# Kernel optimization log

Hardware: AMD Instinct MI355X
Metric: run time of the kernel (lower is better)

Reference implementation:

```python
import jax, jax.numpy as jnp
import numpy as np

B, S, D, H, DK, DFF = 4, 1024, 1024, 16, 64, 4096
EPS = 1e-5


def layer_norm(x, g, b):
    m = jnp.mean(x, axis=-1, keepdims=True)
    v = jnp.var(x, axis=-1, keepdims=True)
    return (x - m) * jax.lax.rsqrt(v + EPS) * g + b


def setup_inputs() -> dict:
    key = jax.random.key(0)
    ks = jax.random.split(key, 12)
    sc = 0.02
    return {
        "x":    jax.random.normal(ks[0], (B, S, D), jnp.float32),
        # per-head Q/K/V projections, stacked over heads: [H, D, DK]
        "Wq":   jax.random.normal(ks[1], (H, D, DK), jnp.float32) * sc,
        "bq":   jnp.zeros((H, DK), jnp.float32),
        "Wk":   jax.random.normal(ks[2], (H, D, DK), jnp.float32) * sc,
        "bk":   jnp.zeros((H, DK), jnp.float32),
        "Wv":   jax.random.normal(ks[3], (H, D, DK), jnp.float32) * sc,
        "bv":   jnp.zeros((H, DK), jnp.float32),
        # output projection: [H*DK, D]
        "Wo":   jax.random.normal(ks[4], (H * DK, D), jnp.float32) * sc,
        "bo":   jnp.zeros((D,), jnp.float32),
        # FFN
        "W1":   jax.random.normal(ks[5], (D, DFF), jnp.float32) * sc,
        "b1":   jnp.zeros((DFF,), jnp.float32),
        "W2":   jax.random.normal(ks[6], (DFF, D), jnp.float32) * sc,
        "b2":   jnp.zeros((D,), jnp.float32),
        # LayerNorms
        "g1":   jnp.ones((D,), jnp.float32),
        "be1":  jnp.zeros((D,), jnp.float32),
        "g2":   jnp.ones((D,), jnp.float32),
        "be2":  jnp.zeros((D,), jnp.float32),
    }


def reference(x, Wq, bq, Wk, bk, Wv, bv, Wo, bo, W1, b1, W2, b2, g1, be1, g2, be2):
    # batched multi-head attention (original loops per head; math identical)
    q = jnp.einsum("bsd,hdk->bhsk", x, Wq) + bq[None, :, None, :]
    k = jnp.einsum("bsd,hdk->bhsk", x, Wk) + bk[None, :, None, :]
    v = jnp.einsum("bsd,hdk->bhsk", x, Wv) + bv[None, :, None, :]
    scale = 1.0 / jnp.sqrt(jnp.asarray(DK, x.dtype))
    scores = jnp.einsum("bhsk,bhtk->bhst", q * scale, k)
    attn = jax.nn.softmax(scores, axis=-1)  # dropout = eval-mode identity
    o = jnp.einsum("bhst,bhtk->bhsk", attn, v)
    # torch.cat over heads along dim 2 -> [B, S, H*DK]
    o = jnp.transpose(o, (0, 2, 1, 3)).reshape(B, S, H * DK)
    att = o @ Wo + bo
    # post-attn: residual of LayerNorm(att)
    x = x + layer_norm(att, g1, be1)
    # FFN
    pos = jax.nn.relu(x @ W1 + b1) @ W2 + b2
    x = x + layer_norm(pos, g2, be2)
    return x
```

## Files before the change

### kernel.cpp

```cpp
#include <hip/hip_runtime.h>
#include <hip/hip_bf16.h>
#include <hip/hip_fp16.h>

typedef unsigned short u16;
typedef short bf16x8_t __attribute__((ext_vector_type(8)));
typedef float f32x4_t  __attribute__((ext_vector_type(4)));

__device__ __forceinline__ u16 f2bf(float f) {
    __hip_bfloat16 h = __float2bfloat16(f);
    union { __hip_bfloat16 b; u16 u; } cv; cv.b = h; return cv.u;
}

__device__ __forceinline__ float bf2f(u16 u) {
    union { unsigned int w; float f; } cv; cv.w = (unsigned int)u << 16; return cv.f;
}

__device__ __forceinline__ void g2l16(const void* g, void* l) {
    __builtin_amdgcn_global_load_lds(
        (const __attribute__((address_space(1))) unsigned int*)g,
        (__attribute__((address_space(3))) unsigned int*)l, 16, 0, 0);
}

__global__ __launch_bounds__(256)
void k_prep(const float* __restrict__ x, u16* __restrict__ Xb,
            const float* __restrict__ Wq, const float* __restrict__ Wk,
            const float* __restrict__ Wv, u16* __restrict__ Wqkvt,
            const float* __restrict__ Wo, const float* __restrict__ W1,
            const float* __restrict__ W2, u16* __restrict__ Wot,
            u16* __restrict__ W1t, u16* __restrict__ W2t)
{
    int id = blockIdx.x;
    if (id < 4096) {
        int i = id * 256 + threadIdx.x;
        float4 f = ((const float4*)x)[i];
        ushort4 o;
        o.x = f2bf(f.x); o.y = f2bf(f.y); o.z = f2bf(f.z); o.w = f2bf(f.w);
        ((ushort4*)Xb)[i] = o;
        return;
    }
    id -= 4096;
    const float* in; u16* out; int R, C, r0, c0;
    if (id < 768) {
        int zx = id >> 8, hy = (id >> 4) & 15, tx = id & 15;
        in  = (zx == 0 ? Wq : (zx == 1 ? Wk : Wv)) + (size_t)hy * 65536;
        out = Wqkvt + ((size_t)zx * 1024 + hy * 64) * 1024;
        R = 1024; C = 64; r0 = tx * 64; c0 = 0;
    } else {
        id -= 768;
        int tx, ty;
        if (id < 256)       { in = Wo; out = Wot; R = 1024; C = 1024; tx = id & 15; ty = id >> 4; }
        else if (id < 1280) { id -= 256; in = W1; out = W1t; R = 1024; C = 4096; tx = id & 63; ty = id >> 6; }
        else                { id -= 1280; in = W2; out = W2t; R = 4096; C = 1024; tx = id & 15; ty = id >> 4; }
        r0 = ty * 64; c0 = tx * 64;
    }
    __shared__ float t[64][65];
    int lc = threadIdx.x & 63, lr = threadIdx.x >> 6;
#pragma unroll
    for (int p = 0; p < 16; ++p) {
        int rr = p * 4 + lr;
        t[rr][lc] = in[(size_t)(r0 + rr) * C + c0 + lc];
    }
    __syncthreads();
#pragma unroll
    for (int p = 0; p < 16; ++p) {
        int cc = p * 4 + lr;
        out[(size_t)(c0 + cc) * R + r0 + lc] = f2bf(t[lc][cc]);
    }
}

__global__ __launch_bounds__(256, 4)
void k_gemm_bt(const u16* __restrict__ A, const u16* __restrict__ Bt,
               void* __restrict__ out, int M, int N, int K, int kchunk)
{
    __shared__ __align__(16) u16 As[2 * 128 * 32];
    __shared__ __align__(16) u16 Bs[2 * 128 * 32];
    int tid = threadIdx.x;
    int wave = tid >> 6, lane = tid & 63;

    int nx = gridDim.x, nwg = nx * gridDim.y;
    int f  = blockIdx.x + nx * blockIdx.y;
    int f2 = (f & 7) * (nwg >> 3) + (f >> 3);
    int bx = f2 % nx, by = f2 / nx;
    int row0 = by * 128, col0 = bx * 128;

    int z = blockIdx.z;
    int kbeg = z * kchunk;

    int lrow = lane >> 2, lcol = (lane & 3) * 8;
    const u16* pA0 = A  + (size_t)(row0 + wave * 16 + lrow) * K + kbeg + lcol;
    const u16* pA1 = pA0 + (size_t)64 * K;
    const u16* pB0 = Bt + (size_t)(col0 + wave * 16 + lrow) * K + kbeg + lcol;
    const u16* pB1 = pB0 + (size_t)64 * K;
    u16* lA0 = &As[wave * 512];
    u16* lA1 = &As[2048 + wave * 512];
    u16* lB0 = &Bs[wave * 512];
    u16* lB1 = &Bs[2048 + wave * 512];

    int wm = (wave >> 1) * 64, wn = (wave & 1) * 64;
    int quad = lane >> 4, l16 = lane & 15;

    f32x4_t acc[4][4];
#pragma unroll
    for (int i = 0; i < 4; i++)
#pragma unroll
        for (int j = 0; j < 4; j++) acc[i][j] = f32x4_t{0.f, 0.f, 0.f, 0.f};

    for (int kk = 0; kk < kchunk; kk += 64) {
        __syncthreads();
        g2l16(pA0, lA0);      g2l16(pA1, lA1);
        g2l16(pA0 + 32, lA0 + 4096); g2l16(pA1 + 32, lA1 + 4096);
        g2l16(pB0, lB0);      g2l16(pB1, lB1);
        g2l16(pB0 + 32, lB0 + 4096); g2l16(pB1 + 32, lB1 + 4096);
        pA0 += 64; pA1 += 64; pB0 += 64; pB1 += 64;
        __syncthreads();

#pragma unroll
        for (int s = 0; s < 2; ++s) {
            const u16* as = &As[s * 4096];
            const u16* bs = &Bs[s * 4096];
            bf16x8_t a[4], b[4];
#pragma unroll
            for (int i = 0; i < 4; ++i)
                a[i] = *(const bf16x8_t*)&as[(wm + i * 16 + l16) * 32 + quad * 8];
#pragma unroll
            for (int j = 0; j < 4; ++j)
                b[j] = *(const bf16x8_t*)&bs[(wn + j * 16 + l16) * 32 + quad * 8];
#pragma unroll
            for (int i = 0; i < 4; ++i)
#pragma unroll
                for (int j = 0; j < 4; ++j)
                    acc[i][j] = __builtin_amdgcn_mfma_f32_16x16x32_bf16(a[i], b[j], acc[i][j], 0, 0, 0);
        }
    }

#pragma unroll
    for (int i = 0; i < 4; ++i)
#pragma unroll
        for (int j = 0; j < 4; ++j)
#pragma unroll
            for (int r = 0; r < 4; ++r) {
                int row = row0 + wm + i * 16 + quad * 4 + r;
                int col = col0 + wn + j * 16 + l16;
                ((__half*)out)[(size_t)z * M * N + (size_t)row * N + col] =
                    __float2half(acc[i][j][r]);
            }
}

template<int EPI>
__device__ __forceinline__
void gemm256x128(const u16* __restrict__ A, const u16* __restrict__ Bt,
                 const float* __restrict__ bias0, void* __restrict__ out,
                 int M, int N, int K, int kchunk, int z, int bx, int by)
{
    __shared__ __align__(16) u16 As[2 * 256 * 32];
    __shared__ __align__(16) u16 Bs[2 * 128 * 32];
    int tid = threadIdx.x;
    int wave = tid >> 6, lane = tid & 63;
    int row0 = by * 256, col0 = bx * 128;
    int kbeg = z * kchunk;

    int lrow = lane >> 2, lcol = (lane & 3) * 8;
    const u16* pA0 = A  + (size_t)(row0 + wave * 16 + lrow) * K + kbeg + lcol;
    const u16* pA1 = pA0 + (size_t)128 * K;
    const u16* pB0 = Bt + (size_t)(col0 + wave * 16 + lrow) * K + kbeg + lcol;
    u16* lA0 = &As[wave * 512];
    u16* lA1 = &As[4096 + wave * 512];
    u16* lB0 = &Bs[wave * 512];

    int wm = (wave >> 1) * 64, wn = (wave & 1) * 64;
    int quad = lane >> 4, l16 = lane & 15;

    f32x4_t acc[4][4];
#pragma unroll
    for (int i = 0; i < 4; i++)
#pragma unroll
        for (int j = 0; j < 4; j++) acc[i][j] = f32x4_t{0.f, 0.f, 0.f, 0.f};

    for (int kk = 0; kk < kchunk; kk += 64) {
        __syncthreads();
        g2l16(pA0, lA0);           g2l16(pA1, lA1);
        g2l16(pA0 + 32, lA0 + 8192); g2l16(pA1 + 32, lA1 + 8192);
        g2l16(pB0, lB0);           g2l16(pB0 + 32, lB0 + 4096);
        pA0 += 64; pA1 += 64; pB0 += 64;
        __syncthreads();

#pragma unroll
        for (int s = 0; s < 2; ++s) {
            const u16* as = &As[s * 8192];
            const u16* bs = &Bs[s * 4096];
            bf16x8_t a[4], b[4];
#pragma unroll
            for (int i = 0; i < 4; ++i)
                a[i] = *(const bf16x8_t*)&as[(wm + i * 16 + l16) * 32 + quad * 8];
#pragma unroll
            for (int j = 0; j < 4; ++j)
                b[j] = *(const bf16x8_t*)&bs[(wn + j * 16 + l16) * 32 + quad * 8];
#pragma unroll
            for (int i = 0; i < 4; ++i)
#pragma unroll
                for (int j = 0; j < 4; ++j)
                    acc[i][j] = __builtin_amdgcn_mfma_f32_16x16x32_bf16(a[i], b[j], acc[i][j], 0, 0, 0);
        }
    }

#pragma unroll
    for (int i = 0; i < 4; ++i)
#pragma unroll
        for (int j = 0; j < 4; ++j)
#pragma unroll
            for (int r = 0; r < 4; ++r) {
                int row = row0 + wm + i * 16 + quad * 4 + r;
                int col = col0 + wn + j * 16 + l16;
                float v = acc[i][j][r];
                if (EPI == 0) {
                    ((__half*)out)[(size_t)z * M * N + (size_t)row * N + col] = __float2half(v);
                } else {
                    ((u16*)out)[(size_t)row * N + col] = f2bf(fmaxf(v + bias0[col], 0.f));
                }
            }
}

__global__ __launch_bounds__(256, 4)
void k_gemm_qkv(const u16* __restrict__ A, const u16* __restrict__ Bt,
                const float* __restrict__ bq, const float* __restrict__ bk,
                const float* __restrict__ bv, u16* __restrict__ QK,
                u16* __restrict__ VT, int M, int N, int K)
{
    __shared__ __align__(16) char pool[34816];
    u16* As = (u16*)pool;
    u16* Bs = (u16*)(pool + 16384);

    int tid = threadIdx.x;
    int wave = tid >> 6, lane = tid & 63;

    int nx = gridDim.x, nwg = nx * gridDim.y;
    int f  = blockIdx.x + nx * blockIdx.y;
    int f2 = (f & 7) * (nwg >> 3) + (f >> 3);
    int bx = f2 % nx, by = f2 / nx;
    int row0 = by * 128, col0 = bx * 128;

    int lrow = lane >> 2, lcol = (lane & 3) * 8;
    const u16* pA0 = A  + (size_t)(row0 + wave * 16 + lrow) * K + lcol;
    const u16* pA1 = pA0 + (size_t)64 * K;
    const u16* pB0 = Bt + (size_t)(col0 + wave * 16 + lrow) * K + lcol;
    const u16* pB1 = pB0 + (size_t)64 * K;
    u16* lA0 = As + wave * 512;
    u16* lA1 = As + 2048 + wave * 512;
    u16* lB0 = Bs + wave * 512;
    u16* lB1 = Bs + 2048 + wave * 512;

    int wm = (wave >> 1) * 64, wn = (wave & 1) * 64;
    int quad = lane >> 4, l16 = lane & 15;

    f32x4_t acc[4][4];
#pragma unroll
    for (int i = 0; i < 4; i++)
#pragma unroll
        for (int j = 0; j < 4; j++) acc[i][j] = f32x4_t{0.f, 0.f, 0.f, 0.f};

    for (int kk = 0; kk < K; kk += 64) {
        __syncthreads();
        g2l16(pA0, lA0);      g2l16(pA1, lA1);
        g2l16(pA0 + 32, lA0 + 4096); g2l16(pA1 + 32, lA1 + 4096);
        g2l16(pB0, lB0);      g2l16(pB1, lB1);
        g2l16(pB0 + 32, lB0 + 4096); g2l16(pB1 + 32, lB1 + 4096);
        pA0 += 64; pA1 += 64; pB0 += 64; pB1 += 64;
        __syncthreads();

#pragma unroll
        for (int s = 0; s < 2; ++s) {
            const u16* as = As + s * 4096;
            const u16* bs = Bs + s * 4096;
            bf16x8_t a[4], b[4];
#pragma unroll
            for (int i = 0; i < 4; ++i)
                a[i] = *(const bf16x8_t*)(as + (wm + i * 16 + l16) * 32 + quad * 8);
#pragma unroll
            for (int j = 0; j < 4; ++j)
                b[j] = *(const bf16x8_t*)(bs + (wn + j * 16 + l16) * 32 + quad * 8);
#pragma unroll
            for (int i = 0; i < 4; ++i)
#pragma unroll
                for (int j = 0; j < 4; ++j)
                    acc[i][j] = __builtin_amdgcn_mfma_f32_16x16x32_bf16(a[i], b[j], acc[i][j], 0, 0, 0);
        }
    }

    int proj = col0 >> 10;
    int h0   = (col0 & 1023) >> 6;
    int b_   = row0 >> 10, sb = row0 & 1023;

    if (proj < 2) {
        const float* bp = proj == 0 ? bq : bk;
        float scale = proj == 0 ? 0.18033688f : 1.f;
        u16* dstbase = QK + (size_t)proj * 4194304;
#pragma unroll
        for (int i = 0; i < 4; ++i)
#pragma unroll
            for (int j = 0; j < 4; ++j)
#pragma unroll
                for (int r = 0; r < 4; ++r) {
                    int row = row0 + wm + i * 16 + quad * 4 + r;
                    int col = col0 + wn + j * 16 + l16;
                    int within = col & 1023;
                    float v = (acc[i][j][r] + bp[within]) * scale;
                    int h = within >> 6, kq = within & 63;
                    int s_ = row & 1023;
                    size_t bh = (size_t)((b_ << 4) + h);
                    dstbase[bh * 65536 + ((size_t)s_ << 6) + kq] = f2bf(v);
                }
    } else {
        u16* tile = (u16*)pool;
        __syncthreads();
#pragma unroll
        for (int i = 0; i < 4; ++i)
#pragma unroll
            for (int j = 0; j < 4; ++j) {
                int c = wn + j * 16 + l16;
                int bcol = (col0 & 1023) + c;
#pragma unroll
                for (int r = 0; r < 4; ++r)
                    tile[c * 136 + wm + i * 16 + quad * 4 + r] =
                        f2bf(acc[i][j][r] + bv[bcol]);
            }
        __syncthreads();
        int c = tid >> 1, v0 = (tid & 1) * 8;
        int head = c >> 6, kq = c & 63;
        size_t bh = (size_t)(b_ * 16 + h0 + head);
        u16* vb = VT + bh * 65536 + (size_t)kq * 1024 + sb;
#pragma unroll
        for (int k = 0; k < 8; ++k) {
            uint4 x = *(const uint4*)&tile[c * 136 + (v0 + k) * 8];
            *(uint4*)&vb[(v0 + k) * 8] = x;
        }
    }
}

__global__ __launch_bounds__(512, 4)
void k_gemm_ffn1(const u16* __restrict__ A, const u16* __restrict__ Bt,
                 const float* __restrict__ b1, void* __restrict__ out,
                 int M, int N, int K)
{
    int nx = gridDim.x, nwg = nx * gridDim.y;
    int f  = blockIdx.x + nx * blockIdx.y;
    int f2 = (f & 7) * (nwg >> 3) + (f >> 3);
    gemm256x128<1>(A, Bt, b1, out, M, N, K, K, 0, f2 % nx, f2 / nx);
}

__global__ __launch_bounds__(512, 4)
void k_gemm_ffn2(const u16* __restrict__ A, const u16* __restrict__ Bt,
                 void* __restrict__ out, int M, int N, int K, int kchunk)
{
    int nx = gridDim.x, nwg = nx * gridDim.y;
    int f  = blockIdx.x + nx * blockIdx.y;
    int f2 = (f & 7) * (nwg >> 3) + (f >> 3);
    gemm256x128<0>(A, Bt, nullptr, out, M, N, K, kchunk, blockIdx.z, f2 % nx, f2 / nx);
}

__global__ __launch_bounds__(512, 4)
void k_attn(const u16* __restrict__ Qg, const u16* __restrict__ Kg,
            const u16* __restrict__ VTg, u16* __restrict__ Og)
{
    __shared__ __align__(16) u16 Ks[2][64 * 64];
    __shared__ __align__(16) u16 Vs[2][64 * 64];
    __shared__ __align__(16) u16 Ps[128 * 64];

    int tid = threadIdx.x, wave = tid >> 6, lane = tid & 63;
    int quad = lane >> 4, l16 = lane & 15;

    int f  = blockIdx.x + gridDim.x * blockIdx.y;
    int f2 = (f & 7) * ((gridDim.x * gridDim.y) >> 3) + (f >> 3);
    int bh = f2 >> 3;
    int q0 = (f2 & 7) * 128;
    int wrow = wave * 16;

    const u16* Qp  = Qg  + (size_t)bh * 65536;
    const u16* Kp  = Kg  + (size_t)bh * 65536;
    const u16* VTp = VTg + (size_t)bh * 65536;

    int arow_g = q0 + wrow + l16;
    bf16x8_t aq0 = *(const bf16x8_t*)&Qp[(size_t)arow_g * 64 + quad * 8];
    bf16x8_t aq1 = *(const bf16x8_t*)&Qp[(size_t)arow_g * 64 + 32 + quad * 8];

    int srow = tid >> 3, scb = tid & 7;
    int sdoff = srow * 64 + ((scb ^ (srow & 7)) * 8);

    uint4 kreg = *(const uint4*)&Kp[(size_t)srow * 64 + scb * 8];
    uint4 vreg = *(const uint4*)&VTp[(size_t)srow * 1024 + scb * 8];

    f32x4_t o[4], lsum;
#pragma unroll
    for (int nt = 0; nt < 4; ++nt) o[nt] = f32x4_t{0.f, 0.f, 0.f, 0.f};
    lsum = f32x4_t{0.f, 0.f, 0.f, 0.f};

    bf16x8_t ones;
#pragma unroll
    for (int j = 0; j < 8; ++j) ones[j] = (short)0x3F80;

    int a7 = l16 & 7;

    *(uint4*)&Ks[0][sdoff] = kreg;
    *(uint4*)&Vs[0][sdoff] = vreg;
    kreg = *(const uint4*)&Kp[(size_t)(64 + srow) * 64 + scb * 8];
    vreg = *(const uint4*)&VTp[(size_t)srow * 1024 + 64 + scb * 8];
    __syncthreads();

    for (int t = 0; t < 16; ++t) {
        int cur = t & 1, nxt = cur ^ 1;
        if (t < 15) {
            *(uint4*)&Ks[nxt][sdoff] = kreg;
            *(uint4*)&Vs[nxt][sdoff] = vreg;
        }
        if (t < 14) {
            kreg = *(const uint4*)&Kp[(size_t)((t + 2) * 64 + srow) * 64 + scb * 8];
            vreg = *(const uint4*)&VTp[(size_t)srow * 1024 + (t + 2) * 64 + scb * 8];
        }

        f32x4_t s[4];
        __builtin_amdgcn_s_setprio(1);
#pragma unroll
        for (int nt = 0; nt < 4; ++nt) {
            int brow = nt * 16 + l16;
            bf16x8_t bk0 = *(const bf16x8_t*)&Ks[cur][brow * 64 + ((quad ^ a7) * 8)];
            bf16x8_t bk1 = *(const bf16x8_t*)&Ks[cur][brow * 64 + (((4 + quad) ^ a7) * 8)];
            s[nt] = __builtin_amdgcn_mfma_f32_16x16x32_bf16(aq0, bk0, f32x4_t{0.f,0.f,0.f,0.f}, 0, 0, 0);
            s[nt] = __builtin_amdgcn_mfma_f32_16x16x32_bf16(aq1, bk1, s[nt], 0, 0, 0);
        }
        __builtin_amdgcn_s_setprio(0);

#pragma unroll
        for (int nt = 0; nt < 4; ++nt) {
            int pcb = nt * 2 + (l16 >> 3);
#pragma unroll
            for (int r = 0; r < 4; ++r) {
                float p = exp2f(s[nt][r]);
                int pr = wrow + quad * 4 + r;
                Ps[pr * 64 + ((pcb ^ (pr & 7)) * 8) + (l16 & 7)] = f2bf(p);
            }
        }

        int arow = wrow + l16;
        bf16x8_t ap0 = *(const bf16x8_t*)&Ps[arow * 64 + ((quad ^ a7) * 8)];
        bf16x8_t ap1 = *(const bf16x8_t*)&Ps[arow * 64 + (((4 + quad) ^ a7) * 8)];
        __builtin_amdgcn_s_setprio(1);
#pragma unroll
        for (int nt = 0; nt < 4; ++nt) {
            int vrow = nt * 16 + l16;
            bf16x8_t bv0 = *(const bf16x8_t*)&Vs[cur][vrow * 64 + ((quad ^ a7) * 8)];
            bf16x8_t bv1 = *(const bf16x8_t*)&Vs[cur][vrow * 64 + (((4 + quad) ^ a7) * 8)];
            o[nt] = __builtin_amdgcn_mfma_f32_16x16x32_bf16(ap0, bv0, o[nt], 0, 0, 0);
            o[nt] = __builtin_amdgcn_mfma_f32_16x16x32_bf16(ap1, bv1, o[nt], 0, 0, 0);
        }
        lsum = __builtin_amdgcn_mfma_f32_16x16x32_bf16(ap0, ones, lsum, 0, 0, 0);
        lsum = __builtin_amdgcn_mfma_f32_16x16x32_bf16(ap1, ones, lsum, 0, 0, 0);
        __builtin_amdgcn_s_setprio(0);
        __syncthreads();
    }

    int b = bh >> 4, h = bh & 15;
    float invl[4];
#pragma unroll
    for (int r = 0; r < 4; ++r) invl[r] = 1.f / lsum[r];
#pragma unroll
    for (int nt = 0; nt < 4; ++nt)
#pragma unroll
        for (int r = 0; r < 4; ++r) {
            int srow2 = q0 + wrow + quad * 4 + r;
            Og[(size_t)(b * 1024 + srow2) * 1024 + (h << 6) + nt * 16 + l16] = f2bf(o[nt][r] * invl[r]);
        }
}

template<int MODE, int NP>
__global__ __launch_bounds__(256)
void k_ln2(const __half* __restrict__ p, const float* __restrict__ bias,
           const float* __restrict__ residf, const u16* __restrict__ residb,
           const float* __restrict__ g, const float* __restrict__ be,
           float* __restrict__ out, u16* __restrict__ outb)
{
    int row = blockIdx.x, tid = threadIdx.x;
    size_t base = (size_t)row * 1024;
    int c0 = tid * 4;
    float xv[4];
    {
        float4 b4 = *(const float4*)&bias[c0];
        xv[0] = b4.x; xv[1] = b4.y; xv[2] = b4.z; xv[3] = b4.w;
    }
#pragma unroll
    for (int z = 0; z < NP; ++z) {
        union { uint2 u; __half h[4]; } cv;
        cv.u = *(const uint2*)&p[(size_t)z * 4194304 + base + c0];
#pragma unroll
        for (int i = 0; i < 4; ++i) xv[i] += __half2float(cv.h[i]);
    }
    float s = 0.f, sq = 0.f;
#pragma unroll
    for (int i = 0; i < 4; ++i) { s += xv[i]; sq += xv[i] * xv[i]; }
#pragma unroll
    for (int off = 32; off; off >>= 1) { s += __shfl_down(s, off); sq += __shfl_down(sq, off); }
    __shared__ float ss[4], ssq[4];
    int wv = tid >> 6;
    if ((tid & 63) == 0) { ss[wv] = s; ssq[wv] = sq; }
    __syncthreads();
    s  = ss[0] + ss[1] + ss[2] + ss[3];
    sq = ssq[0] + ssq[1] + ssq[2] + ssq[3];
    float mean = s * (1.f / 1024.f);
    float var  = sq * (1.f / 1024.f) - mean * mean;
    float rstd = rsqrtf(var + 1e-5f);

    float4 g4  = *(const float4*)&g[c0];
    float4 be4 = *(const float4*)&be[c0];
    float gv[4] = {g4.x, g4.y, g4.z, g4.w};
    float bv[4] = {be4.x, be4.y, be4.z, be4.w};
    float rv[4];
    if (MODE == 0) {
        float4 r4 = *(const float4*)&residf[base + c0];
        rv[0] = r4.x; rv[1] = r4.y; rv[2] = r4.z; rv[3] = r4.w;
    } else {
        ushort4 rb = *(const ushort4*)&residb[base + c0];
        rv[0] = bf2f(rb.x); rv[1] = bf2f(rb.y); rv[2] = bf2f(rb.z); rv[3] = bf2f(rb.w);
    }
    float y[4];
#pragma unroll
    for (int i = 0; i < 4; ++i) y[i] = rv[i] + (xv[i] - mean) * rstd * gv[i] + bv[i];
    if (MODE == 0) {
        ushort4 o;
        o.x = f2bf(y[0]); o.y = f2bf(y[1]); o.z = f2bf(y[2]); o.w = f2bf(y[3]);
        *(ushort4*)&outb[base + c0] = o;
    } else {
        float4 o; o.x = y[0]; o.y = y[1]; o.z = y[2]; o.w = y[3];
        *(float4*)&out[base + c0] = o;
    }
}

extern "C" void kernel_launch(void* const* d_in, const int* in_sizes, int n_in,
                              void* d_out, int out_size, void* d_ws, size_t ws_size,
                              hipStream_t stream) {
    const float* x   = (const float*)d_in[0];
    const float* Wq  = (const float*)d_in[1];
    const float* bq  = (const float*)d_in[2];
    const float* Wk  = (const float*)d_in[3];
    const float* bk  = (const float*)d_in[4];
    const float* Wv  = (const float*)d_in[5];
    const float* bv  = (const float*)d_in[6];
    const float* Wo  = (const float*)d_in[7];
    const float* bo  = (const float*)d_in[8];
    const float* W1  = (const float*)d_in[9];
    const float* b1  = (const float*)d_in[10];
    const float* W2  = (const float*)d_in[11];
    const float* b2  = (const float*)d_in[12];
    const float* g1  = (const float*)d_in[13];
    const float* be1 = (const float*)d_in[14];
    const float* g2  = (const float*)d_in[15];
    const float* be2 = (const float*)d_in[16];
    float* out = (float*)d_out;

    char* w = (char*)d_ws;
    u16*    Xb    = (u16*)(w);
    u16*    Wqkvt = (u16*)(w + 8388608);
    u16*    Wot   = (u16*)(w + 14680064);
    u16*    W1t   = (u16*)(w + 16777216);
    u16*    W2t   = (u16*)(w + 25165824);
    u16*    Qb    = (u16*)(w + 33554432);
    u16*    VTb   = (u16*)(w + 50331648);
    u16*    Oc    = (u16*)(w + 58720256);
    __half* part4 = (__half*)(w + 33554432);
    __half* part2 = (__half*)(w + 67108864);
    u16*    x1b   = (u16*)(w + 117440512);
    u16*    hb    = (u16*)(w + 125829120);

    k_prep<<<7168, 256, 0, stream>>>(x, Xb, Wq, Wk, Wv, Wqkvt, Wo, W1, W2, Wot, W1t, W2t);

    k_gemm_qkv<<<dim3(24, 32), 256, 0, stream>>>(Xb, Wqkvt, bq, bk, bv, Qb, VTb, 4096, 3072, 1024);

    k_attn<<<dim3(8, 64), 512, 0, stream>>>(Qb, Qb + 4194304, VTb, Oc);

    k_gemm_bt<<<dim3(8, 32, 2), 256, 0, stream>>>(Oc, Wot, part2, 4096, 1024, 1024, 512);

    k_ln2<0, 2><<<4096, 256, 0, stream>>>(part2, bo, x, nullptr, g1, be1, nullptr, x1b);

    k_gemm_ffn1<<<dim3(32, 16), 512, 0, stream>>>(x1b, W1t, b1, hb, 4096, 4096, 1024);

    k_gemm_ffn2<<<dim3(8, 16, 4), 512, 0, stream>>>(hb, W2t, part4, 4096, 1024, 4096, 1024);

    k_ln2<1, 4><<<4096, 256, 0, stream>>>(part4, b2, nullptr, x1b, g2, be2, out, nullptr);
}
```

Before: 303.6 us.

## Process two 16-row query groups per wave in attention kernel with 256 threads

The attention kernel drops from 8 waves to 4 waves per block, and each wave now handles 32 query rows as two 16-row groups. Each K/V fragment read from LDS is reused for two MFMA groups, which halves LDS read traffic per unit of compute. Each thread now stages two K and two V rows per tile. The costs are higher register pressure, a launch bound relaxed to (256, 2), and fewer waves available to hide latency.

```diff
diff --git a/kernel.cpp b/kernel.cpp
--- a/kernel.cpp
+++ b/kernel.cpp
@@ -357,7 +357,7 @@
     gemm256x128<0>(A, Bt, nullptr, out, M, N, K, kchunk, blockIdx.z, f2 % nx, f2 / nx);
 }
 
-__global__ __launch_bounds__(512, 4)
+__global__ __launch_bounds__(256, 2)
 void k_attn(const u16* __restrict__ Qg, const u16* __restrict__ Kg,
             const u16* __restrict__ VTg, u16* __restrict__ Og)
 {
@@ -372,26 +372,37 @@
     int f2 = (f & 7) * ((gridDim.x * gridDim.y) >> 3) + (f >> 3);
     int bh = f2 >> 3;
     int q0 = (f2 & 7) * 128;
-    int wrow = wave * 16;
+    int wrow = wave * 32;
 
     const u16* Qp  = Qg  + (size_t)bh * 65536;
     const u16* Kp  = Kg  + (size_t)bh * 65536;
     const u16* VTp = VTg + (size_t)bh * 65536;
 
-    int arow_g = q0 + wrow + l16;
-    bf16x8_t aq0 = *(const bf16x8_t*)&Qp[(size_t)arow_g * 64 + quad * 8];
-    bf16x8_t aq1 = *(const bf16x8_t*)&Qp[(size_t)arow_g * 64 + 32 + quad * 8];
+    bf16x8_t aq[2][2];
+#pragma unroll
+    for (int g = 0; g < 2; ++g) {
+        int arow_g = q0 + wrow + g * 16 + l16;
+        aq[g][0] = *(const bf16x8_t*)&Qp[(size_t)arow_g * 64 + quad * 8];
+        aq[g][1] = *(const bf16x8_t*)&Qp[(size_t)arow_g * 64 + 32 + quad * 8];
+    }
 
     int srow = tid >> 3, scb = tid & 7;
-    int sdoff = srow * 64 + ((scb ^ (srow & 7)) * 8);
-
-    uint4 kreg = *(const uint4*)&Kp[(size_t)srow * 64 + scb * 8];
-    uint4 vreg = *(const uint4*)&VTp[(size_t)srow * 1024 + scb * 8];
-
-    f32x4_t o[4], lsum;
-#pragma unroll
-    for (int nt = 0; nt < 4; ++nt) o[nt] = f32x4_t{0.f, 0.f, 0.f, 0.f};
-    lsum = f32x4_t{0.f, 0.f, 0.f, 0.f};
+    int srow2 = srow + 32;
+    int sdoff0 = srow  * 64 + ((scb ^ (srow  & 7)) * 8);
+    int sdoff1 = srow2 * 64 + ((scb ^ (srow2 & 7)) * 8);
+
+    uint4 kreg0 = *(const uint4*)&Kp[(size_t)srow  * 64 + scb * 8];
+    uint4 kreg1 = *(const uint4*)&Kp[(size_t)srow2 * 64 + scb * 8];
+    uint4 vreg0 = *(const uint4*)&VTp[(size_t)srow  * 1024 + scb * 8];
+    uint4 vreg1 = *(const uint4*)&VTp[(size_t)srow2 * 1024 + scb * 8];
+
+    f32x4_t o[2][4], lsum[2];
+#pragma unroll
+    for (int g = 0; g < 2; ++g) {
+#pragma unroll
+        for (int nt = 0; nt < 4; ++nt) o[g][nt] = f32x4_t{0.f, 0.f, 0.f, 0.f};
+        lsum[g] = f32x4_t{0.f, 0.f, 0.f, 0.f};
+    }
 
     bf16x8_t ones;
 #pragma unroll
@@ -399,75 +410,98 @@
 
     int a7 = l16 & 7;
 
-    *(uint4*)&Ks[0][sdoff] = kreg;
-    *(uint4*)&Vs[0][sdoff] = vreg;
-    kreg = *(const uint4*)&Kp[(size_t)(64 + srow) * 64 + scb * 8];
-    vreg = *(const uint4*)&VTp[(size_t)srow * 1024 + 64 + scb * 8];
+    *(uint4*)&Ks[0][sdoff0] = kreg0;  *(uint4*)&Ks[0][sdoff1] = kreg1;
+    *(uint4*)&Vs[0][sdoff0] = vreg0;  *(uint4*)&Vs[0][sdoff1] = vreg1;
+    kreg0 = *(const uint4*)&Kp[(size_t)(64 + srow ) * 64 + scb * 8];
+    kreg1 = *(const uint4*)&Kp[(size_t)(64 + srow2) * 64 + scb * 8];
+    vreg0 = *(const uint4*)&VTp[(size_t)srow  * 1024 + 64 + scb * 8];
+    vreg1 = *(const uint4*)&VTp[(size_t)srow2 * 1024 + 64 + scb * 8];
     __syncthreads();
 
     for (int t = 0; t < 16; ++t) {
         int cur = t & 1, nxt = cur ^ 1;
         if (t < 15) {
-            *(uint4*)&Ks[nxt][sdoff] = kreg;
-            *(uint4*)&Vs[nxt][sdoff] = vreg;
+            *(uint4*)&Ks[nxt][sdoff0] = kreg0;  *(uint4*)&Ks[nxt][sdoff1] = kreg1;
+            *(uint4*)&Vs[nxt][sdoff0] = vreg0;  *(uint4*)&Vs[nxt][sdoff1] = vreg1;
         }
         if (t < 14) {
-            kreg = *(const uint4*)&Kp[(size_t)((t + 2) * 64 + srow) * 64 + scb * 8];
-            vreg = *(const uint4*)&VTp[(size_t)srow * 1024 + (t + 2) * 64 + scb * 8];
-        }
-
-        f32x4_t s[4];
+            kreg0 = *(const uint4*)&Kp[(size_t)((t + 2) * 64 + srow ) * 64 + scb * 8];
+            kreg1 = *(const uint4*)&Kp[(size_t)((t + 2) * 64 + srow2) * 64 + scb * 8];
+            vreg0 = *(const uint4*)&VTp[(size_t)srow  * 1024 + (t + 2) * 64 + scb * 8];
+            vreg1 = *(const uint4*)&VTp[(size_t)srow2 * 1024 + (t + 2) * 64 + scb * 8];
+        }
+
+        f32x4_t s[2][4];
         __builtin_amdgcn_s_setprio(1);
 #pragma unroll
         for (int nt = 0; nt < 4; ++nt) {
             int brow = nt * 16 + l16;
             bf16x8_t bk0 = *(const bf16x8_t*)&Ks[cur][brow * 64 + ((quad ^ a7) * 8)];
             bf16x8_t bk1 = *(const bf16x8_t*)&Ks[cur][brow * 64 + (((4 + quad) ^ a7) * 8)];
-            s[nt] = __builtin_amdgcn_mfma_f32_16x16x32_bf16(aq0, bk0, f32x4_t{0.f,0.f,0.f,0.f}, 0, 0, 0);
-            s[nt] = __builtin_amdgcn_mfma_f32_16x16x32_bf16(aq1, bk1, s[nt], 0, 0, 0);
+#pragma unroll
+            for (int g = 0; g < 2; ++g) {
+                s[g][nt] = __builtin_amdgcn_mfma_f32_16x16x32_bf16(aq[g][0], bk0, f32x4_t{0.f,0.f,0.f,0.f}, 0, 0, 0);
+                s[g][nt] = __builtin_amdgcn_mfma_f32_16x16x32_bf16(aq[g][1], bk1, s[g][nt], 0, 0, 0);
+            }
         }
         __builtin_amdgcn_s_setprio(0);
 
 #pragma unroll
-        for (int nt = 0; nt < 4; ++nt) {
-            int pcb = nt * 2 + (l16 >> 3);
-#pragma unroll
-            for (int r = 0; r < 4; ++r) {
-                float p = exp2f(s[nt][r]);
-                int pr = wrow + quad * 4 + r;
-                Ps[pr * 64 + ((pcb ^ (pr & 7)) * 8) + (l16 & 7)] = f2bf(p);
+        for (int g = 0; g < 2; ++g)
+#pragma unroll
+            for (int nt = 0; nt < 4; ++nt) {
+                int pcb = nt * 2 + (l16 >> 3);
+#pragma unroll
+                for (int r = 0; r < 4; ++r) {
+                    float p = exp2f(s[g][nt][r]);
+                    int pr = wrow + g * 16 + quad * 4 + r;
+                    Ps[pr * 64 + ((pcb ^ (pr & 7)) * 8) + (l16 & 7)] = f2bf(p);
+                }
             }
-        }
-
-        int arow = wrow + l16;
-        bf16x8_t ap0 = *(const bf16x8_t*)&Ps[arow * 64 + ((quad ^ a7) * 8)];
-        bf16x8_t ap1 = *(const bf16x8_t*)&Ps[arow * 64 + (((4 + quad) ^ a7) * 8)];
+
+        bf16x8_t ap[2][2];
+#pragma unroll
+        for (int g = 0; g < 2; ++g) {
+            int arow = wrow + g * 16 + l16;
+            ap[g][0] = *(const bf16x8_t*)&Ps[arow * 64 + ((quad ^ a7) * 8)];
+            ap[g][1] = *(const bf16x8_t*)&Ps[arow * 64 + (((4 + quad) ^ a7) * 8)];
+        }
         __builtin_amdgcn_s_setprio(1);
 #pragma unroll
         for (int nt = 0; nt < 4; ++nt) {
             int vrow = nt * 16 + l16;
             bf16x8_t bv0 = *(const bf16x8_t*)&Vs[cur][vrow * 64 + ((quad ^ a7) * 8)];
             bf16x8_t bv1 = *(const bf16x8_t*)&Vs[cur][vrow * 64 + (((4 + quad) ^ a7) * 8)];
-            o[nt] = __builtin_amdgcn_mfma_f32_16x16x32_bf16(ap0, bv0, o[nt], 0, 0, 0);
-            o[nt] = __builtin_amdgcn_mfma_f32_16x16x32_bf16(ap1, bv1, o[nt], 0, 0, 0);
-        }
-        lsum = __builtin_amdgcn_mfma_f32_16x16x32_bf16(ap0, ones, lsum, 0, 0, 0);
-        lsum = __builtin_amdgcn_mfma_f32_16x16x32_bf16(ap1, ones, lsum, 0, 0, 0);
+#pragma unroll
+            for (int g = 0; g < 2; ++g) {
+                o[g][nt] = __builtin_amdgcn_mfma_f32_16x16x32_bf16(ap[g][0], bv0, o[g][nt], 0, 0, 0);
+                o[g][nt] = __builtin_amdgcn_mfma_f32_16x16x32_bf16(ap[g][1], bv1, o[g][nt], 0, 0, 0);
+            }
+        }
+#pragma unroll
+        for (int g = 0; g < 2; ++g) {
+            lsum[g] = __builtin_amdgcn_mfma_f32_16x16x32_bf16(ap[g][0], ones, lsum[g], 0, 0, 0);
+            lsum[g] = __builtin_amdgcn_mfma_f32_16x16x32_bf16(ap[g][1], ones, lsum[g], 0, 0, 0);
+        }
         __builtin_amdgcn_s_setprio(0);
         __syncthreads();
     }
 
     int b = bh >> 4, h = bh & 15;
-    float invl[4];
-#pragma unroll
-    for (int r = 0; r < 4; ++r) invl[r] = 1.f / lsum[r];
-#pragma unroll
-    for (int nt = 0; nt < 4; ++nt)
-#pragma unroll
-        for (int r = 0; r < 4; ++r) {
-            int srow2 = q0 + wrow + quad * 4 + r;
-            Og[(size_t)(b * 1024 + srow2) * 1024 + (h << 6) + nt * 16 + l16] = f2bf(o[nt][r] * invl[r]);
-        }
+#pragma unroll
+    for (int g = 0; g < 2; ++g) {
+        float invl[4];
+#pragma unroll
+        for (int r = 0; r < 4; ++r) invl[r] = 1.f / lsum[g][r];
+#pragma unroll
+        for (int nt = 0; nt < 4; ++nt)
+#pragma unroll
+            for (int r = 0; r < 4; ++r) {
+                int srow_o = q0 + wrow + g * 16 + quad * 4 + r;
+                Og[(size_t)(b * 1024 + srow_o) * 1024 + (h << 6) + nt * 16 + l16] =
+                    f2bf(o[g][nt][r] * invl[r]);
+            }
+    }
 }
 
 template<int MODE, int NP>
@@ -572,7 +606,7 @@
 
     k_gemm_qkv<<<dim3(24, 32), 256, 0, stream>>>(Xb, Wqkvt, bq, bk, bv, Qb, VTb, 4096, 3072, 1024);
 
-    k_attn<<<dim3(8, 64), 512, 0, stream>>>(Qb, Qb + 4194304, VTb, Oc);
+    k_attn<<<dim3(8, 64), 256, 0, stream>>>(Qb, Qb + 4194304, VTb, Oc);
 
     k_gemm_bt<<<dim3(8, 32, 2), 256, 0, stream>>>(Oc, Wot, part2, 4096, 1024, 1024, 512);
 
```

New measurement: 302.8 us. Within noise of the previous version (-0.3%).
